# Optimization experiments

Hardware: AMD Instinct MI355X
Metric: run time of the kernel (lower is better)

## Reference

```python
import jax, jax.numpy as jnp
import numpy as np

N = 100000
F_IN = 1433
H1, H2 = 32, 16
E = 3200000


def gcn_conv(x, W, b, src, dst, deg_isqrt):
    # PyG GCNConv: h = x @ W; out[dst] += norm * h[src]; out += b
    h = x @ W                                  # [N, out]
    norm = deg_isqrt[src] * deg_isqrt[dst]     # [E+N]
    msg = norm[:, None] * h[src]               # gather [E+N, out]
    out = jax.ops.segment_sum(msg, dst, num_segments=N)
    return out + b


def setup_inputs() -> dict:
    key = jax.random.key(0)
    ks = jax.random.split(key, 8)
    x = jax.random.normal(ks[0], (N, F_IN), dtype=jnp.float32)
    edge_index = jax.random.randint(ks[1], (2, E), 0, N, dtype=jnp.int64)
    s1 = 1.0 / np.sqrt(F_IN)
    s2 = 1.0 / np.sqrt(H1)
    s3 = 1.0 / np.sqrt(H2)
    W1 = jax.random.uniform(ks[2], (F_IN, H1), jnp.float32, -s1, s1)
    b1 = jnp.zeros((H1,), jnp.float32)
    W2 = jax.random.uniform(ks[3], (H1, H2), jnp.float32, -s2, s2)
    b2 = jnp.zeros((H2,), jnp.float32)
    Wl = jax.random.uniform(ks[4], (H2, F_IN), jnp.float32, -s3, s3)
    bl = jax.random.uniform(ks[5], (F_IN,), jnp.float32, -s3, s3)
    return {"x": x, "W1": W1, "b1": b1, "W2": W2, "b2": b2,
            "Wl": Wl, "bl": bl, "edge_index": edge_index}


def reference(x, W1, b1, W2, b2, Wl, bl, edge_index):
    # add self-loops (as PyG GCNConv does by default)
    loop = jnp.arange(N, dtype=edge_index.dtype)
    src = jnp.concatenate([edge_index[0], loop])
    dst = jnp.concatenate([edge_index[1], loop])
    # symmetric normalization deg^{-1/2} with self-loops included
    deg = jax.ops.segment_sum(jnp.ones_like(dst, dtype=x.dtype), dst, num_segments=N)
    deg_isqrt = jnp.where(deg > 0, jax.lax.rsqrt(deg), 0.0)

    h = jax.nn.relu(gcn_conv(x, W1, b1, src, dst, deg_isqrt))
    # dropout is a no-op in eval mode
    h = jax.nn.relu(gcn_conv(h, W2, b2, src, dst, deg_isqrt))
    out = h @ Wl + bl                          # [N, F_IN]
    return jax.nn.log_softmax(out, axis=1)
```

## Files before the change

kernel.cpp:

```cpp
#include <hip/hip_runtime.h>
#include <hip/hip_bf16.h>

#define N_NODES 100000
#define F_IN 1433
#define H1F 32
#define H2F 16
#define NBLK_SCAN 98

typedef __bf16 bf16x8 __attribute__((ext_vector_type(8)));
typedef float f32x4 __attribute__((ext_vector_type(4)));

#define O_H1ACC 0
#define O_H2ACC 3200000
#define O_CNT   4800000
#define O_LSE   4900000
#define O_H1PRE 5000000
#define O_H2PRE 8200000
#define O_DISQ  9800000
#define O_WLT   9900000
#define O_W1F   9924000

__global__ void k_deg(const int* __restrict__ dst, int E, int* __restrict__ cnt) {
    int t = blockIdx.x * 256 + threadIdx.x;
    if (t < E) atomicAdd(&cnt[dst[t]], 1);
}

__global__ void k_disq(const int* __restrict__ cnt, float* __restrict__ disq) {
    int t = blockIdx.x * 256 + threadIdx.x;
    if (t < N_NODES) disq[t] = rsqrtf((float)(cnt[t] + 1));
}

__global__ __launch_bounds__(256) void k_scansum(const int* __restrict__ cnt,
                                                 int* __restrict__ bsum) {
    __shared__ int lds[256];
    int t = threadIdx.x, b = blockIdx.x;
    int i = b * 1024 + t * 4;
    int c0 = 0, c1 = 0, c2 = 0, c3 = 0;
    if (i + 3 < N_NODES) {
        int4 v = *(const int4*)(cnt + i);
        c0 = v.x; c1 = v.y; c2 = v.z; c3 = v.w;
    } else {
        if (i + 0 < N_NODES) c0 = cnt[i + 0];
        if (i + 1 < N_NODES) c1 = cnt[i + 1];
        if (i + 2 < N_NODES) c2 = cnt[i + 2];
        if (i + 3 < N_NODES) c3 = cnt[i + 3];
    }
    lds[t] = c0 + c1 + c2 + c3;
    __syncthreads();
    for (int off = 128; off > 0; off >>= 1) {
        if (t < off) lds[t] += lds[t + off];
        __syncthreads();
    }
    if (t == 0) bsum[b] = lds[0];
}

__global__ __launch_bounds__(128) void k_scanbase(const int* __restrict__ bsum,
                                                  int* __restrict__ bbase,
                                                  int* __restrict__ rowptr) {
    __shared__ int lds[128];
    int t = threadIdx.x;
    lds[t] = (t < NBLK_SCAN) ? bsum[t] : 0;
    __syncthreads();
    for (int off = 1; off < 128; off <<= 1) {
        int u = (t >= off) ? lds[t - off] : 0;
        __syncthreads();
        lds[t] += u;
        __syncthreads();
    }
    bbase[t] = (t == 0) ? 0 : lds[t - 1];
    if (t == NBLK_SCAN - 1) rowptr[N_NODES] = lds[t];
}

__global__ __launch_bounds__(256) void k_scanwrite(const int* __restrict__ cnt,
                                                   const int* __restrict__ bbase,
                                                   int* __restrict__ rowptr,
                                                   int* __restrict__ fill) {
    __shared__ int lds[256];
    int t = threadIdx.x, b = blockIdx.x;
    int i = b * 1024 + t * 4;
    int c0 = 0, c1 = 0, c2 = 0, c3 = 0;
    if (i + 3 < N_NODES) {
        int4 v = *(const int4*)(cnt + i);
        c0 = v.x; c1 = v.y; c2 = v.z; c3 = v.w;
    } else {
        if (i + 0 < N_NODES) c0 = cnt[i + 0];
        if (i + 1 < N_NODES) c1 = cnt[i + 1];
        if (i + 2 < N_NODES) c2 = cnt[i + 2];
        if (i + 3 < N_NODES) c3 = cnt[i + 3];
    }
    int s = c0 + c1 + c2 + c3;
    lds[t] = s;
    __syncthreads();
    for (int off = 1; off < 256; off <<= 1) {
        int u = (t >= off) ? lds[t - off] : 0;
        __syncthreads();
        lds[t] += u;
        __syncthreads();
    }
    int p = bbase[b] + lds[t] - s;
    if (i + 0 < N_NODES) { rowptr[i + 0] = p; fill[i + 0] = p; p += c0; }
    if (i + 1 < N_NODES) { rowptr[i + 1] = p; fill[i + 1] = p; p += c1; }
    if (i + 2 < N_NODES) { rowptr[i + 2] = p; fill[i + 2] = p; p += c2; }
    if (i + 3 < N_NODES) { rowptr[i + 3] = p; fill[i + 3] = p; p += c3; }
}

__global__ void k_fill(const int* __restrict__ src, const int* __restrict__ dst, int E,
                       int* __restrict__ fill, int* __restrict__ csr) {
    int t = blockIdx.x * 256 + threadIdx.x;
    if (t < E) {
        int slot = atomicAdd(&fill[dst[t]], 1);
        csr[slot] = src[t];
    }
}

__global__ void k_w1f(const float* __restrict__ W1, __bf16* __restrict__ w1f) {
    int t = blockIdx.x * 256 + threadIdx.x;
    if (t >= 45 * 1024) return;
    int j = t & 7, lane = (t >> 3) & 63, nt = (t >> 9) & 1, ks = t >> 10;
    int k = ks * 32 + (lane >> 4) * 8 + j;
    int f = nt * 16 + (lane & 15);
    float v = (k < F_IN) ? W1[k * H1F + f] : 0.f;
    w1f[t] = (__bf16)v;
}

__global__ void k_wlt(const float* __restrict__ Wl, float* __restrict__ wlt) {
    int t = blockIdx.x * 256 + threadIdx.x;
    if (t < F_IN * H2F) {
        int j = t >> 4, k = t & 15;
        wlt[t] = Wl[k * F_IN + j];
    }
}

__global__ __launch_bounds__(256) void k_gemm1(const float* __restrict__ x,
                                               const __bf16* __restrict__ w1f,
                                               float* __restrict__ h1pre) {
    const int lane = threadIdx.x & 63;
    const int wv   = threadIdx.x >> 6;
    const int l16  = lane & 15, quad = lane >> 4;
    const int rowb = blockIdx.x * 128 + wv * 32;
    const long r0 = min(rowb + l16, N_NODES - 1);
    const long r1 = min(rowb + 16 + l16, N_NODES - 1);
    const float* xr0 = x + r0 * F_IN;
    const float* xr1 = x + r1 * F_IN;
    f32x4 acc00 = {0,0,0,0}, acc01 = {0,0,0,0}, acc10 = {0,0,0,0}, acc11 = {0,0,0,0};
    const bf16x8* bfp = (const bf16x8*)w1f;

    for (int ks = 0; ks < 45; ks++) {
        int kb = ks * 32 + quad * 8;
        bf16x8 a0, a1;
#pragma unroll
        for (int j = 0; j < 8; j++) {
            int k = kb + j; k = k > (F_IN - 1) ? (F_IN - 1) : k;
            a0[j] = (__bf16)xr0[k];
            a1[j] = (__bf16)xr1[k];
        }
        bf16x8 b0 = bfp[(ks * 2 + 0) * 64 + lane];
        bf16x8 b1 = bfp[(ks * 2 + 1) * 64 + lane];
        acc00 = __builtin_amdgcn_mfma_f32_16x16x32_bf16(a0, b0, acc00, 0, 0, 0);
        acc01 = __builtin_amdgcn_mfma_f32_16x16x32_bf16(a0, b1, acc01, 0, 0, 0);
        acc10 = __builtin_amdgcn_mfma_f32_16x16x32_bf16(a1, b0, acc10, 0, 0, 0);
        acc11 = __builtin_amdgcn_mfma_f32_16x16x32_bf16(a1, b1, acc11, 0, 0, 0);
    }
#pragma unroll
    for (int reg = 0; reg < 4; reg++) {
        int m0 = rowb + quad * 4 + reg;
        int m1 = m0 + 16;
        if (m0 < N_NODES) {
            h1pre[(long)m0 * 32 + l16]      = acc00[reg];
            h1pre[(long)m0 * 32 + 16 + l16] = acc01[reg];
        }
        if (m1 < N_NODES) {
            h1pre[(long)m1 * 32 + l16]      = acc10[reg];
            h1pre[(long)m1 * 32 + 16 + l16] = acc11[reg];
        }
    }
}

__global__ __launch_bounds__(256) void k_agg1(const int* __restrict__ rowptr,
                                              const int* __restrict__ csr,
                                              const float* __restrict__ disq,
                                              const float* __restrict__ h1pre,
                                              const float* __restrict__ b1,
                                              float* __restrict__ h1) {
    int t = blockIdx.x * 256 + threadIdx.x;
    int n = t >> 3, q = t & 7;
    if (n >= N_NODES) return;
    int e0 = rowptr[n], e1 = rowptr[n + 1];
    float4 acc = {0.f, 0.f, 0.f, 0.f};
    for (int e = e0; e < e1; e++) {
        int s = csr[e];
        float w = disq[s];
        float4 v = ((const float4*)(h1pre + (long)s * 32))[q];
        acc.x += w * v.x; acc.y += w * v.y; acc.z += w * v.z; acc.w += w * v.w;
    }
    float dq = disq[n];
    float4 self = ((const float4*)(h1pre + (long)n * 32))[q];
    float4 bb = ((const float4*)b1)[q];
    float4 r;
    r.x = fmaxf(dq * acc.x + dq * dq * self.x + bb.x, 0.f);
    r.y = fmaxf(dq * acc.y + dq * dq * self.y + bb.y, 0.f);
    r.z = fmaxf(dq * acc.z + dq * dq * self.z + bb.z, 0.f);
    r.w = fmaxf(dq * acc.w + dq * dq * self.w + bb.w, 0.f);
    ((float4*)(h1 + (long)n * 32))[q] = r;
}

__global__ void k_gemm2(const float* __restrict__ h1, const float* __restrict__ W2,
                        float* __restrict__ h2pre) {
    int t = blockIdx.x * 256 + threadIdx.x;
    if (t >= N_NODES * 16) return;
    int n = t >> 4, f = t & 15;
    const float4* hv = (const float4*)(h1 + (long)n * 32);
    float acc = 0.f;
#pragma unroll
    for (int kq = 0; kq < 8; kq++) {
        float4 h = hv[kq];
        acc += h.x * W2[(kq * 4 + 0) * 16 + f] + h.y * W2[(kq * 4 + 1) * 16 + f]
             + h.z * W2[(kq * 4 + 2) * 16 + f] + h.w * W2[(kq * 4 + 3) * 16 + f];
    }
    h2pre[t] = acc;
}

__global__ __launch_bounds__(256) void k_agg2(const int* __restrict__ rowptr,
                                              const int* __restrict__ csr,
                                              const float* __restrict__ disq,
                                              const float* __restrict__ h2pre,
                                              const float* __restrict__ b2,
                                              float* __restrict__ h2) {
    int t = blockIdx.x * 256 + threadIdx.x;
    int n = t >> 2, q = t & 3;
    if (n >= N_NODES) return;
    int e0 = rowptr[n], e1 = rowptr[n + 1];
    float4 acc = {0.f, 0.f, 0.f, 0.f};
    for (int e = e0; e < e1; e++) {
        int s = csr[e];
        float w = disq[s];
        float4 v = ((const float4*)(h2pre + (long)s * 16))[q];
        acc.x += w * v.x; acc.y += w * v.y; acc.z += w * v.z; acc.w += w * v.w;
    }
    float dq = disq[n];
    float4 self = ((const float4*)(h2pre + (long)n * 16))[q];
    float4 bb = ((const float4*)b2)[q];
    float4 r;
    r.x = fmaxf(dq * acc.x + dq * dq * self.x + bb.x, 0.f);
    r.y = fmaxf(dq * acc.y + dq * dq * self.y + bb.y, 0.f);
    r.z = fmaxf(dq * acc.z + dq * dq * self.z + bb.z, 0.f);
    r.w = fmaxf(dq * acc.w + dq * dq * self.w + bb.w, 0.f);
    ((float4*)(h2 + (long)n * 16))[q] = r;
}

__global__ __launch_bounds__(256) void k_stats(const float* __restrict__ h2,
                                               const float* __restrict__ wlt,
                                               const float* __restrict__ bl,
                                               float* __restrict__ lseacc) {
    int wv = threadIdx.x >> 6, lane = threadIdx.x & 63;
    int jc = blockIdx.x;
    int nw = blockIdx.y * 4 + wv;
    int j0 = jc * 180, j1 = min(j0 + 180, F_IN);
    int nb = nw * 256 + lane;
    float hr[4][16];
    float acc[4] = {0.f, 0.f, 0.f, 0.f};
#pragma unroll
    for (int i = 0; i < 4; i++) {
        long n = min(nb + 64 * i, N_NODES - 1);
        const float4* hv = (const float4*)(h2 + n * 16);
#pragma unroll
        for (int q = 0; q < 4; q++) {
            float4 h = hv[q];
            hr[i][q * 4 + 0] = h.x; hr[i][q * 4 + 1] = h.y;
            hr[i][q * 4 + 2] = h.z; hr[i][q * 4 + 3] = h.w;
        }
    }
    for (int j = j0; j < j1; j++) {
        const float4* wv4 = (const float4*)(wlt + j * 16);
        float wk[16];
#pragma unroll
        for (int q = 0; q < 4; q++) {
            float4 w = wv4[q];
            wk[q * 4 + 0] = w.x; wk[q * 4 + 1] = w.y; wk[q * 4 + 2] = w.z; wk[q * 4 + 3] = w.w;
        }
        float b = bl[j];
#pragma unroll
        for (int i = 0; i < 4; i++) {
            float lg = b;
#pragma unroll
            for (int k = 0; k < 16; k++) lg += hr[i][k] * wk[k];
            acc[i] += __expf(lg);
        }
    }
#pragma unroll
    for (int i = 0; i < 4; i++) {
        int n = nb + 64 * i;
        if (n < N_NODES) unsafeAtomicAdd(&lseacc[n], acc[i]);
    }
}

__global__ void k_lse(float* __restrict__ lse) {
    int t = blockIdx.x * 256 + threadIdx.x;
    if (t < N_NODES) lse[t] = __logf(lse[t]);
}

__global__ __launch_bounds__(256) void k_passb(const float* __restrict__ h2,
                                               const float* __restrict__ Wl,
                                               const float* __restrict__ bl,
                                               const float* __restrict__ lse,
                                               float* __restrict__ out) {
    int wv = threadIdx.x >> 6, lane = threadIdx.x & 63;
    int tile = blockIdx.x;
    float wf[4][16], bias[4];
    int cols[4]; bool cv[4];
#pragma unroll
    for (int c = 0; c < 4; c++) {
        int col = tile * 256 + c * 64 + lane;
        cv[c] = col < F_IN;
        int cc = min(col, F_IN - 1);
        cols[c] = cc;
        bias[c] = bl[cc];
#pragma unroll
        for (int k = 0; k < 16; k++) wf[c][k] = Wl[k * F_IN + cc];
    }
    int n0 = (blockIdx.y * 4 + wv) * 128;
    for (int i = 0; i < 128; i++) {
        int n = n0 + i;
        if (n >= N_NODES) break;
        const float4* hv = (const float4*)(h2 + (long)n * 16);
        float4 h0 = hv[0], h1v = hv[1], h2v = hv[2], h3v = hv[3];
        float l = lse[n];
        float* op = out + (long)n * F_IN;
#pragma unroll
        for (int c = 0; c < 4; c++) {
            float lg = bias[c]
                + h0.x * wf[c][0]  + h0.y * wf[c][1]  + h0.z * wf[c][2]  + h0.w * wf[c][3]
                + h1v.x * wf[c][4] + h1v.y * wf[c][5] + h1v.z * wf[c][6] + h1v.w * wf[c][7]
                + h2v.x * wf[c][8] + h2v.y * wf[c][9] + h2v.z * wf[c][10]+ h2v.w * wf[c][11]
                + h3v.x * wf[c][12]+ h3v.y * wf[c][13]+ h3v.z * wf[c][14]+ h3v.w * wf[c][15];
            if (cv[c]) op[cols[c]] = lg - l;
        }
    }
}

extern "C" void kernel_launch(void* const* d_in, const int* in_sizes, int n_in,
                              void* d_out, int out_size, void* d_ws, size_t ws_size,
                              hipStream_t stream) {
    const float* x  = (const float*)d_in[0];
    const float* W1 = (const float*)d_in[1];
    const float* b1 = (const float*)d_in[2];
    const float* W2 = (const float*)d_in[3];
    const float* b2 = (const float*)d_in[4];
    const float* Wl = (const float*)d_in[5];
    const float* bl = (const float*)d_in[6];
    const int*   ei = (const int*)d_in[7];
    const int E = in_sizes[7] / 2;
    const int* srcp = ei;
    const int* dstp = ei + E;

    float* ws    = (float*)d_ws;
    float* h1    = ws + O_H1ACC;
    float* h2    = ws + O_H2ACC;
    int*   cnt   = (int*)(ws + O_CNT);
    float* lse   = ws + O_LSE;
    float* h1pre = ws + O_H1PRE;
    float* h2pre = ws + O_H2PRE;
    float* disq  = ws + O_DISQ;
    float* wlt   = ws + O_WLT;
    __bf16* w1f  = (__bf16*)(ws + O_W1F);
    float* out   = (float*)d_out;

    int* csr    = (int*)d_out;
    int* rowptr = csr + E;
    int* fill   = rowptr + N_NODES + 1;
    int* bsum   = fill + N_NODES;
    int* bbase  = bsum + 128;

    hipMemsetAsync(ws + O_CNT, 0, 200000 * sizeof(float), stream);

    k_deg<<<(E + 255) / 256, 256, 0, stream>>>(dstp, E, cnt);
    k_disq<<<(N_NODES + 255) / 256, 256, 0, stream>>>(cnt, disq);
    k_w1f<<<(45 * 1024 + 255) / 256, 256, 0, stream>>>(W1, w1f);
    k_wlt<<<(F_IN * H2F + 255) / 256, 256, 0, stream>>>(Wl, wlt);

    k_scansum<<<NBLK_SCAN, 256, 0, stream>>>(cnt, bsum);
    k_scanbase<<<1, 128, 0, stream>>>(bsum, bbase, rowptr);
    k_scanwrite<<<NBLK_SCAN, 256, 0, stream>>>(cnt, bbase, rowptr, fill);
    k_fill<<<(E + 255) / 256, 256, 0, stream>>>(srcp, dstp, E, fill, csr);

    k_gemm1<<<(N_NODES + 127) / 128, 256, 0, stream>>>(x, w1f, h1pre);
    k_agg1<<<(N_NODES * 8 + 255) / 256, 256, 0, stream>>>(rowptr, csr, disq, h1pre, b1, h1);

    k_gemm2<<<(N_NODES * 16 + 255) / 256, 256, 0, stream>>>(h1, W2, h2pre);
    k_agg2<<<(N_NODES * 4 + 255) / 256, 256, 0, stream>>>(rowptr, csr, disq, h2pre, b2, h2);

    k_stats<<<dim3(8, 98), 256, 0, stream>>>(h2, wlt, bl, lse);
    k_lse<<<(N_NODES + 255) / 256, 256, 0, stream>>>(lse);
    k_passb<<<dim3(6, 196), 256, 0, stream>>>(h2, Wl, bl, lse, out);
}
```

Measured before the change: 2.052 ms.

## Pre-convert x to padded bf16, simplify GEMM1 tiling, unroll aggregation loops

A new pre-pass converts the fp32 feature matrix into a zero-padded bf16 copy with a row stride of 1440, stored in scratch space inside the output buffer. GEMM1 can then load each A fragment as one 16-byte vector with no per-element clamping or conversion; each wave now handles 16 rows instead of 32. The aim is to replace poorly coalesced scalar fp32 loads in the GEMM with a coalesced conversion pass followed by vector loads. The cost is an extra write and read of the bf16 copy. Separately, both neighbour aggregation loops are unrolled by two to keep more gathers in flight.

```diff
diff --git a/kernel.cpp b/kernel.cpp
--- a/kernel.cpp
+++ b/kernel.cpp
@@ -3,6 +3,7 @@
 
 #define N_NODES 100000
 #define F_IN 1433
+#define F_PAD 1440
 #define H1F 32
 #define H2F 16
 #define NBLK_SCAN 98
@@ -19,6 +20,8 @@
 #define O_DISQ  9800000
 #define O_WLT   9900000
 #define O_W1F   9924000
+
+#define XBF_OFF_INT 4000000
 
 __global__ void k_deg(const int* __restrict__ dst, int E, int* __restrict__ cnt) {
     int t = blockIdx.x * 256 + threadIdx.x;
@@ -113,6 +116,17 @@
     }
 }
 
+__global__ __launch_bounds__(256) void k_xbf(const float* __restrict__ x,
+                                             __bf16* __restrict__ xbf) {
+    int row = blockIdx.x;
+    const float* xr = x + (long)row * F_IN;
+    __bf16* o = xbf + (long)row * F_PAD;
+    for (int j = threadIdx.x; j < F_PAD; j += 256) {
+        float v = (j < F_IN) ? xr[j] : 0.f;
+        o[j] = (__bf16)v;
+    }
+}
+
 __global__ void k_w1f(const float* __restrict__ W1, __bf16* __restrict__ w1f) {
     int t = blockIdx.x * 256 + threadIdx.x;
     if (t >= 45 * 1024) return;
@@ -131,47 +145,32 @@
     }
 }
 
-__global__ __launch_bounds__(256) void k_gemm1(const float* __restrict__ x,
+__global__ __launch_bounds__(256) void k_gemm1(const __bf16* __restrict__ xbf,
                                                const __bf16* __restrict__ w1f,
                                                float* __restrict__ h1pre) {
     const int lane = threadIdx.x & 63;
     const int wv   = threadIdx.x >> 6;
     const int l16  = lane & 15, quad = lane >> 4;
-    const int rowb = blockIdx.x * 128 + wv * 32;
-    const long r0 = min(rowb + l16, N_NODES - 1);
-    const long r1 = min(rowb + 16 + l16, N_NODES - 1);
-    const float* xr0 = x + r0 * F_IN;
-    const float* xr1 = x + r1 * F_IN;
-    f32x4 acc00 = {0,0,0,0}, acc01 = {0,0,0,0}, acc10 = {0,0,0,0}, acc11 = {0,0,0,0};
+    const int rowb = blockIdx.x * 64 + wv * 16;
+    const long r = min(rowb + l16, N_NODES - 1);
+    const __bf16* xr = xbf + r * F_PAD + quad * 8;
+    f32x4 acc0 = {0,0,0,0}, acc1 = {0,0,0,0};
     const bf16x8* bfp = (const bf16x8*)w1f;
 
+#pragma unroll 5
     for (int ks = 0; ks < 45; ks++) {
-        int kb = ks * 32 + quad * 8;
-        bf16x8 a0, a1;
-#pragma unroll
-        for (int j = 0; j < 8; j++) {
-            int k = kb + j; k = k > (F_IN - 1) ? (F_IN - 1) : k;
-            a0[j] = (__bf16)xr0[k];
-            a1[j] = (__bf16)xr1[k];
-        }
+        bf16x8 a  = *(const bf16x8*)(xr + ks * 32);
         bf16x8 b0 = bfp[(ks * 2 + 0) * 64 + lane];
         bf16x8 b1 = bfp[(ks * 2 + 1) * 64 + lane];
-        acc00 = __builtin_amdgcn_mfma_f32_16x16x32_bf16(a0, b0, acc00, 0, 0, 0);
-        acc01 = __builtin_amdgcn_mfma_f32_16x16x32_bf16(a0, b1, acc01, 0, 0, 0);
-        acc10 = __builtin_amdgcn_mfma_f32_16x16x32_bf16(a1, b0, acc10, 0, 0, 0);
-        acc11 = __builtin_amdgcn_mfma_f32_16x16x32_bf16(a1, b1, acc11, 0, 0, 0);
+        acc0 = __builtin_amdgcn_mfma_f32_16x16x32_bf16(a, b0, acc0, 0, 0, 0);
+        acc1 = __builtin_amdgcn_mfma_f32_16x16x32_bf16(a, b1, acc1, 0, 0, 0);
     }
 #pragma unroll
     for (int reg = 0; reg < 4; reg++) {
-        int m0 = rowb + quad * 4 + reg;
-        int m1 = m0 + 16;
-        if (m0 < N_NODES) {
-            h1pre[(long)m0 * 32 + l16]      = acc00[reg];
-            h1pre[(long)m0 * 32 + 16 + l16] = acc01[reg];
-        }
-        if (m1 < N_NODES) {
-            h1pre[(long)m1 * 32 + l16]      = acc10[reg];
-            h1pre[(long)m1 * 32 + 16 + l16] = acc11[reg];
+        int m = rowb + quad * 4 + reg;
+        if (m < N_NODES) {
+            h1pre[(long)m * 32 + l16]      = acc0[reg];
+            h1pre[(long)m * 32 + 16 + l16] = acc1[reg];
         }
     }
 }
@@ -187,7 +186,18 @@
     if (n >= N_NODES) return;
     int e0 = rowptr[n], e1 = rowptr[n + 1];
     float4 acc = {0.f, 0.f, 0.f, 0.f};
-    for (int e = e0; e < e1; e++) {
+    int e = e0;
+    for (; e + 1 < e1; e += 2) {
+        int s0 = csr[e], s1 = csr[e + 1];
+        float w0 = disq[s0], w1 = disq[s1];
+        float4 v0 = ((const float4*)(h1pre + (long)s0 * 32))[q];
+        float4 v1 = ((const float4*)(h1pre + (long)s1 * 32))[q];
+        acc.x += w0 * v0.x + w1 * v1.x;
+        acc.y += w0 * v0.y + w1 * v1.y;
+        acc.z += w0 * v0.z + w1 * v1.z;
+        acc.w += w0 * v0.w + w1 * v1.w;
+    }
+    if (e < e1) {
         int s = csr[e];
         float w = disq[s];
         float4 v = ((const float4*)(h1pre + (long)s * 32))[q];
@@ -231,7 +241,18 @@
     if (n >= N_NODES) return;
     int e0 = rowptr[n], e1 = rowptr[n + 1];
     float4 acc = {0.f, 0.f, 0.f, 0.f};
-    for (int e = e0; e < e1; e++) {
+    int e = e0;
+    for (; e + 1 < e1; e += 2) {
+        int s0 = csr[e], s1 = csr[e + 1];
+        float w0 = disq[s0], w1 = disq[s1];
+        float4 v0 = ((const float4*)(h2pre + (long)s0 * 16))[q];
+        float4 v1 = ((const float4*)(h2pre + (long)s1 * 16))[q];
+        acc.x += w0 * v0.x + w1 * v1.x;
+        acc.y += w0 * v0.y + w1 * v1.y;
+        acc.z += w0 * v0.z + w1 * v1.z;
+        acc.w += w0 * v0.w + w1 * v1.w;
+    }
+    if (e < e1) {
         int s = csr[e];
         float w = disq[s];
         float4 v = ((const float4*)(h2pre + (long)s * 16))[q];
@@ -370,6 +391,7 @@
     int* fill   = rowptr + N_NODES + 1;
     int* bsum   = fill + N_NODES;
     int* bbase  = bsum + 128;
+    __bf16* xbf = (__bf16*)((int*)d_out + XBF_OFF_INT);
 
     hipMemsetAsync(ws + O_CNT, 0, 200000 * sizeof(float), stream);
 
@@ -383,7 +405,8 @@
     k_scanwrite<<<NBLK_SCAN, 256, 0, stream>>>(cnt, bbase, rowptr, fill);
     k_fill<<<(E + 255) / 256, 256, 0, stream>>>(srcp, dstp, E, fill, csr);
 
-    k_gemm1<<<(N_NODES + 127) / 128, 256, 0, stream>>>(x, w1f, h1pre);
+    k_xbf<<<N_NODES, 256, 0, stream>>>(x, xbf);
+    k_gemm1<<<(N_NODES + 63) / 64, 256, 0, stream>>>(xbf, w1f, h1pre);
     k_agg1<<<(N_NODES * 8 + 255) / 256, 256, 0, stream>>>(rowptr, csr, disq, h1pre, b1, h1);
 
     k_gemm2<<<(N_NODES * 16 + 255) / 256, 256, 0, stream>>>(h1, W2, h2pre);
```

Measured after the change: 1.969 ms. 4.0% less time.
